# Kernel optimization log

Measured on AMD Instinct MI355X. Metric: run time of the kernel, lower is better.

Reference implementation:

```python
import jax, jax.numpy as jnp
import numpy as np

IN_DIM = 4096
OUT_DIM = 4096
RANK = 8
IN1 = IN2 = OUT1 = OUT2 = 64  # factorize(4096) -> (64, 64)


def setup_inputs() -> dict:
    key = jax.random.key(0)
    k1, k2, k3, k4 = jax.random.split(key, 4)
    x = jax.random.normal(k1, (8, 2048, IN_DIM), dtype=jnp.float32)
    L = jax.random.normal(k2, (OUT1, OUT2, IN1, RANK), dtype=jnp.float32) * 0.05
    R = jax.random.normal(k3, (RANK, OUT2, IN1, IN2), dtype=jnp.float32) * 0.05
    bias = jax.random.normal(k4, (OUT_DIM,), dtype=jnp.float32) * 0.02
    return {"x": x, "L": L, "R": R, "bias": bias}


def reference(x, L, R, bias):
    # Assemble full weight: W[a,b,c,d] = sum_r L[a,b,c,r] * R[r,b,c,d]
    W = jnp.einsum('abcr,rbcd->abcd', L, R).reshape(OUT_DIM, IN_DIM)
    shape = x.shape
    X = x.reshape(-1, IN_DIM)          # [BS, in_dim]
    out = X @ W.T + bias               # addmm(bias, x, W.T)
    return out.reshape(*shape[:-1], OUT_DIM)
```

## Files before the change

kernel.cpp:

```cpp
#include <hip/hip_runtime.h>
#include <hip/hip_bf16.h>

typedef __attribute__((ext_vector_type(8))) short bf16x8;
typedef __attribute__((ext_vector_type(4))) float f32x4;

#define GLDS(g, l) \
  __builtin_amdgcn_global_load_lds((const __attribute__((address_space(1))) void*)(g), \
                                   (__attribute__((address_space(3))) void*)(l), 16, 0, 0)

#define MFMA_BF16 __builtin_amdgcn_mfma_f32_16x16x32_bf16

__global__ __launch_bounds__(256) void k_cvt_bf16(const float* __restrict__ x,
                                                  __hip_bfloat16* __restrict__ y,
                                                  long n8) {
  long stride = (long)gridDim.x * blockDim.x;
  for (long i = (long)blockIdx.x * blockDim.x + threadIdx.x; i < n8; i += stride) {
    const float4* xin = reinterpret_cast<const float4*>(x) + i * 2;
    float4 v0 = xin[0];
    float4 v1 = xin[1];
    union { __hip_bfloat16 h[8]; int4 v; } o;
    o.h[0] = __float2bfloat16(v0.x);
    o.h[1] = __float2bfloat16(v0.y);
    o.h[2] = __float2bfloat16(v0.z);
    o.h[3] = __float2bfloat16(v0.w);
    o.h[4] = __float2bfloat16(v1.x);
    o.h[5] = __float2bfloat16(v1.y);
    o.h[6] = __float2bfloat16(v1.z);
    o.h[7] = __float2bfloat16(v1.w);
    *reinterpret_cast<int4*>(y + i * 8) = o.v;
  }
}

__global__ __launch_bounds__(256) void k_make_w(const float* __restrict__ L,
                                                const float* __restrict__ R,
                                                __hip_bfloat16* __restrict__ W) {
  int o = blockIdx.x;
  int b = o & 63;
  __shared__ float Ls[512];
  Ls[threadIdx.x] = L[(size_t)o * 512 + threadIdx.x];
  Ls[threadIdx.x + 256] = L[(size_t)o * 512 + 256 + threadIdx.x];
  __syncthreads();
  for (int idx = threadIdx.x; idx < 4096; idx += 256) {
    int c = idx >> 6;
    int d = idx & 63;
    float s = 0.f;
#pragma unroll
    for (int r = 0; r < 8; ++r) {
      s += Ls[c * 8 + r] * R[(((size_t)(r * 64 + b) * 64 + c) << 6) + d];
    }
    W[(size_t)o * 4096 + idx] = __float2bfloat16(s);
  }
}

__global__ __launch_bounds__(512, 2) void k_gemm_bt(const __hip_bfloat16* __restrict__ A,
                                                    const __hip_bfloat16* __restrict__ B,
                                                    const float* __restrict__ bias,
                                                    float* __restrict__ C) {
  const int K = 4096, N = 4096, NT = 64;
  __shared__ char lds[131072];
  char* const sAc = lds;
  char* const sBc = lds + 65536;

  const int tid = threadIdx.x;
  const int lane = tid & 63;
  const int wid = tid >> 6;
  const int wr = wid >> 2;
  const int wc = wid & 3;

  const int orig = blockIdx.x;
  const int wg = (orig & 7) * 128 + (orig >> 3);
  const int gm0 = (wg >> 4) * 256;
  const int gn0 = (wg & 15) * 256;

  const int crow = tid >> 3;
  const int scol = ((tid & 7) << 4) ^ ((crow & 7) << 4);
  const int voff = crow * 8192 + scol;
  const int wbase = (tid >> 6) << 10;
  const char* const Ab = (const char*)(A + (size_t)gm0 * K);
  const char* const Bb = (const char*)(B + (size_t)gn0 * K);

#define STAGEA(BUF, TS)                                                      \
  _Pragma("unroll")                                                          \
  for (int j = 0; j < 4; ++j)                                                \
    GLDS(Ab + (size_t)((TS) * 128 + j * 524288) + voff,                      \
         sAc + (BUF) * 32768 + j * 8192 + wbase);

#define STAGEB(BUF, TS)                                                      \
  _Pragma("unroll")                                                          \
  for (int j = 0; j < 4; ++j)                                                \
    GLDS(Bb + (size_t)((TS) * 128 + j * 524288) + voff,                      \
         sBc + (BUF) * 32768 + j * 8192 + wbase);

  const int lr = lane & 15;
  const int lk = lane >> 4;
  const int kx0 = (lk << 4) ^ ((lr & 7) << 4);
  const int kx1 = (64 + (lk << 4)) ^ ((lr & 7) << 4);
  const char* const rA0 = sAc + (((wr << 7) + lr) << 7) + kx0;
  const char* const rA1 = sAc + (((wr << 7) + lr) << 7) + kx1;
  const char* const rB0 = sBc + (((wc << 6) + lr) << 7) + kx0;
  const char* const rB1 = sBc + (((wc << 6) + lr) << 7) + kx1;

#define PREFA(DST, BUF, MOFS)                                                \
  _Pragma("unroll")                                                          \
  for (int m = 0; m < 4; ++m) {                                              \
    DST[m][0] = *(const bf16x8*)(rA0 + (BUF) * 32768 + ((MOFS) + m) * 2048); \
    DST[m][1] = *(const bf16x8*)(rA1 + (BUF) * 32768 + ((MOFS) + m) * 2048); \
  }

#define PREFB(DST, BUF, NOFS)                                                \
  _Pragma("unroll")                                                          \
  for (int n = 0; n < 2; ++n) {                                              \
    DST[n][0] = *(const bf16x8*)(rB0 + (BUF) * 32768 + ((NOFS) + n) * 2048); \
    DST[n][1] = *(const bf16x8*)(rB1 + (BUF) * 32768 + ((NOFS) + n) * 2048); \
  }

#define MFMA8X(AF, BF, MB, NB)                                               \
  _Pragma("unroll")                                                          \
  for (int m = 0; m < 4; ++m) {                                              \
    acc[(MB) + m][(NB) + 0] =                                                \
        MFMA_BF16(AF[m][0], BF[0][0], acc[(MB) + m][(NB) + 0], 0, 0, 0);     \
    acc[(MB) + m][(NB) + 0] =                                                \
        MFMA_BF16(AF[m][1], BF[0][1], acc[(MB) + m][(NB) + 0], 0, 0, 0);     \
    acc[(MB) + m][(NB) + 1] =                                                \
        MFMA_BF16(AF[m][0], BF[1][0], acc[(MB) + m][(NB) + 1], 0, 0, 0);     \
    acc[(MB) + m][(NB) + 1] =                                                \
        MFMA_BF16(AF[m][1], BF[1][1], acc[(MB) + m][(NB) + 1], 0, 0, 0);     \
  }

#define LGKM0 asm volatile("s_waitcnt lgkmcnt(0)" ::: "memory")
#define SBAR0 __builtin_amdgcn_sched_barrier(0)

  f32x4 acc[8][4];
#pragma unroll
  for (int m = 0; m < 8; ++m)
#pragma unroll
    for (int n = 0; n < 4; ++n) acc[m][n] = (f32x4){0.f, 0.f, 0.f, 0.f};

  bf16x8 aX[4][2], aY[4][2], b0[2][2], b2[2][2];

  STAGEA(0, 0) STAGEB(0, 0) STAGEA(1, 1) STAGEB(1, 1)
  asm volatile("s_waitcnt vmcnt(8)" ::: "memory");
  SBAR0;
  __builtin_amdgcn_s_barrier();
  PREFA(aX, 0, 0) PREFB(b0, 0, 0)

#define TILE(BUF, T)                                                         \
  {                                                                          \
    const int tS = ((T) + 2 < NT) ? (T) + 2 : NT - 1;                        \
                                                                     \
    LGKM0; SBAR0;                                                            \
    PREFA(aY, BUF, 4)                                                        \
    SBAR0;                                                                   \
    __builtin_amdgcn_s_setprio(1);                                           \
    MFMA8X(aX, b0, 0, 0)                                                     \
    __builtin_amdgcn_s_setprio(0);                                           \
                                                                     \
    LGKM0; SBAR0;                                                            \
    PREFB(b2, BUF, 2)                                                        \
    SBAR0;                                                                   \
    __builtin_amdgcn_s_setprio(1);                                           \
    MFMA8X(aY, b0, 4, 0)                                                     \
    __builtin_amdgcn_s_setprio(0);                                           \
                                           \
    asm volatile("s_waitcnt lgkmcnt(0) vmcnt(0)" ::: "memory");              \
    SBAR0;                                                                   \
    __builtin_amdgcn_s_barrier();                                            \
    STAGEA(BUF, tS)                                                          \
    PREFB(b0, (BUF) ^ 1, 0)                                                  \
    SBAR0;                                                                   \
    __builtin_amdgcn_s_setprio(1);                                           \
    MFMA8X(aX, b2, 0, 2)                                                     \
    __builtin_amdgcn_s_setprio(0);                                           \
                                           \
    SBAR0;                                                                   \
    STAGEB(BUF, tS)                                                          \
    PREFA(aX, (BUF) ^ 1, 0)                                                  \
    SBAR0;                                                                   \
    __builtin_amdgcn_s_setprio(1);                                           \
    MFMA8X(aY, b2, 4, 2)                                                     \
    __builtin_amdgcn_s_setprio(0);                                           \
  }

  for (int t = 0; t < NT; t += 2) {
    TILE(0, t)
    TILE(1, t + 1)
  }

  const int er = gm0 + (wr << 7) + ((lane >> 4) << 2);
  const int ec = gn0 + (wc << 6) + (lane & 15);
#pragma unroll
  for (int n = 0; n < 4; ++n) {
    const int c = ec + n * 16;
    const float bv = bias[c];
#pragma unroll
    for (int m = 0; m < 8; ++m) {
#pragma unroll
      for (int j = 0; j < 4; ++j) {
        C[(size_t)(er + m * 16 + j) * N + c] = acc[m][n][j] + bv;
      }
    }
  }
}

extern "C" void kernel_launch(void* const* d_in, const int* in_sizes, int n_in,
                              void* d_out, int out_size, void* d_ws, size_t ws_size,
                              hipStream_t stream) {
  const float* x = (const float*)d_in[0];
  const float* L = (const float*)d_in[1];
  const float* R = (const float*)d_in[2];
  const float* bias = (const float*)d_in[3];
  float* out = (float*)d_out;

  __hip_bfloat16* Wb = (__hip_bfloat16*)d_ws;
  __hip_bfloat16* Xb = (__hip_bfloat16*)((char*)d_ws + (size_t)4096 * 4096 * 2);

  const long n8 = (long)16384 * 4096 / 8;
  k_cvt_bf16<<<4096, 256, 0, stream>>>(x, Xb, n8);
  k_make_w<<<4096, 256, 0, stream>>>(L, R, Wb);

  dim3 grid(1024);
  k_gemm_bt<<<grid, 512, 0, stream>>>(Xb, Wb, bias, out);
}
```

Before: 575.8 us.

## Restructure GEMM main loop into four-phase pipeline with split global-to-LDS staging

```diff
diff --git a/kernel.cpp b/kernel.cpp
--- a/kernel.cpp
+++ b/kernel.cpp
@@ -72,24 +72,32 @@
   const int gm0 = (wg >> 4) * 256;
   const int gn0 = (wg & 15) * 256;
 
-  const int crow = tid >> 3;
-  const int scol = ((tid & 7) << 4) ^ ((crow & 7) << 4);
-  const int voff = crow * 8192 + scol;
-  const int wbase = (tid >> 6) << 10;
+  const int sc8 = ((lane & 7) << 4) ^ ((lane >> 3) << 4);
   const char* const Ab = (const char*)(A + (size_t)gm0 * K);
   const char* const Bb = (const char*)(B + (size_t)gn0 * K);
 
-#define STAGEA(BUF, TS)                                                      \
-  _Pragma("unroll")                                                          \
-  for (int j = 0; j < 4; ++j)                                                \
-    GLDS(Ab + (size_t)((TS) * 128 + j * 524288) + voff,                      \
-         sAc + (BUF) * 32768 + j * 8192 + wbase);
-
-#define STAGEB(BUF, TS)                                                      \
-  _Pragma("unroll")                                                          \
-  for (int j = 0; j < 4; ++j)                                                \
-    GLDS(Bb + (size_t)((TS) * 128 + j * 524288) + voff,                      \
-         sBc + (BUF) * 32768 + j * 8192 + wbase);
+  auto STAGE_A = [&](int buf, int kt, int par) {
+#pragma unroll
+    for (int i = 0; i < 2; ++i) {
+      const int u = (wid << 1) + i;
+      const int j = ((u >> 3) << 1) + par;
+      const int rb = u & 7;
+      const int row = (j << 6) + (rb << 3) + (lane >> 3);
+      GLDS(Ab + (size_t)row * 8192 + (size_t)kt * 128 + sc8,
+           sAc + buf * 32768 + j * 8192 + rb * 1024);
+    }
+  };
+  auto STAGE_B = [&](int buf, int kt, int half) {
+#pragma unroll
+    for (int i = 0; i < 2; ++i) {
+      const int u = (wid << 1) + i;
+      const int j = u >> 2;
+      const int rb = u & 3;
+      const int row = (j << 6) + (half << 5) + (rb << 3) + (lane >> 3);
+      GLDS(Bb + (size_t)row * 8192 + (size_t)kt * 128 + sc8,
+           sBc + buf * 32768 + j * 8192 + (half << 12) + (rb << 10));
+    }
+  };
 
   const int lr = lane & 15;
   const int lk = lane >> 4;
@@ -129,6 +137,9 @@
 
 #define LGKM0 asm volatile("s_waitcnt lgkmcnt(0)" ::: "memory")
 #define SBAR0 __builtin_amdgcn_sched_barrier(0)
+#define VMC4 asm volatile("s_waitcnt vmcnt(4)" ::: "memory")
+#define VMC2 asm volatile("s_waitcnt vmcnt(2)" ::: "memory")
+#define VMC0 asm volatile("s_waitcnt vmcnt(0)" ::: "memory")
 
   f32x4 acc[8][4];
 #pragma unroll
@@ -136,55 +147,59 @@
 #pragma unroll
     for (int n = 0; n < 4; ++n) acc[m][n] = (f32x4){0.f, 0.f, 0.f, 0.f};
 
-  bf16x8 aX[4][2], aY[4][2], b0[2][2], b2[2][2];
-
-  STAGEA(0, 0) STAGEB(0, 0) STAGEA(1, 1) STAGEB(1, 1)
-  asm volatile("s_waitcnt vmcnt(8)" ::: "memory");
+  bf16x8 a0[4][2], a1[4][2], bb0[2][2], bb1[2][2];
+
+  STAGE_A(0, 0, 0);
+  STAGE_B(0, 0, 0);
+  STAGE_B(0, 0, 1);
+  STAGE_A(0, 0, 1);
+  VMC0;
   SBAR0;
   __builtin_amdgcn_s_barrier();
-  PREFA(aX, 0, 0) PREFB(b0, 0, 0)
-
-#define TILE(BUF, T)                                                         \
-  {                                                                          \
-    const int tS = ((T) + 2 < NT) ? (T) + 2 : NT - 1;                        \
-                                                                     \
-    LGKM0; SBAR0;                                                            \
-    PREFA(aY, BUF, 4)                                                        \
-    SBAR0;                                                                   \
-    __builtin_amdgcn_s_setprio(1);                                           \
-    MFMA8X(aX, b0, 0, 0)                                                     \
-    __builtin_amdgcn_s_setprio(0);                                           \
-                                                                     \
-    LGKM0; SBAR0;                                                            \
-    PREFB(b2, BUF, 2)                                                        \
-    SBAR0;                                                                   \
-    __builtin_amdgcn_s_setprio(1);                                           \
-    MFMA8X(aY, b0, 4, 0)                                                     \
-    __builtin_amdgcn_s_setprio(0);                                           \
-                                           \
-    asm volatile("s_waitcnt lgkmcnt(0) vmcnt(0)" ::: "memory");              \
-    SBAR0;                                                                   \
-    __builtin_amdgcn_s_barrier();                                            \
-    STAGEA(BUF, tS)                                                          \
-    PREFB(b0, (BUF) ^ 1, 0)                                                  \
-    SBAR0;                                                                   \
-    __builtin_amdgcn_s_setprio(1);                                           \
-    MFMA8X(aX, b2, 0, 2)                                                     \
-    __builtin_amdgcn_s_setprio(0);                                           \
-                                           \
-    SBAR0;                                                                   \
-    STAGEB(BUF, tS)                                                          \
-    PREFA(aX, (BUF) ^ 1, 0)                                                  \
-    SBAR0;                                                                   \
-    __builtin_amdgcn_s_setprio(1);                                           \
-    MFMA8X(aY, b2, 4, 2)                                                     \
-    __builtin_amdgcn_s_setprio(0);                                           \
-  }
-
-  for (int t = 0; t < NT; t += 2) {
-    TILE(0, t)
-    TILE(1, t + 1)
-  }
+
+  for (int t = 0; t < NT; ++t) {
+    const int buf = t & 1, nb = buf ^ 1;
+    const bool more = (t + 1 < NT);
+
+    PREFA(a0, buf, 0) PREFB(bb0, buf, 0)
+    if (more) { STAGE_A(nb, t + 1, 0); VMC4; } else { VMC2; }
+    SBAR0;
+    __builtin_amdgcn_s_barrier();
+    LGKM0; SBAR0;
+    __builtin_amdgcn_s_setprio(1);
+    MFMA8X(a0, bb0, 0, 0)
+    __builtin_amdgcn_s_setprio(0);
+    __builtin_amdgcn_s_barrier();
+
+    PREFB(bb1, buf, 2)
+    if (more) { STAGE_B(nb, t + 1, 0); VMC4; } else { VMC0; }
+    SBAR0;
+    __builtin_amdgcn_s_barrier();
+    LGKM0; SBAR0;
+    __builtin_amdgcn_s_setprio(1);
+    MFMA8X(a0, bb1, 0, 2)
+    __builtin_amdgcn_s_setprio(0);
+    __builtin_amdgcn_s_barrier();
+
+    PREFA(a1, buf, 4)
+    if (more) STAGE_B(nb, t + 1, 1);
+    SBAR0;
+    __builtin_amdgcn_s_barrier();
+    LGKM0; SBAR0;
+    __builtin_amdgcn_s_setprio(1);
+    MFMA8X(a1, bb1, 4, 2)
+    __builtin_amdgcn_s_setprio(0);
+    __builtin_amdgcn_s_barrier();
+
+    if (more) { STAGE_A(nb, t + 1, 1); VMC4; }
+    SBAR0;
+    __builtin_amdgcn_s_barrier();
+    __builtin_amdgcn_s_setprio(1);
+    MFMA8X(a1, bb0, 4, 0)
+    __builtin_amdgcn_s_setprio(0);
+    __builtin_amdgcn_s_barrier();
+  }
+  asm volatile("s_waitcnt vmcnt(0) lgkmcnt(0)" ::: "memory");
 
   const int er = gm0 + (wr << 7) + ((lane >> 4) << 2);
   const int ec = gn0 + (wc << 6) + (lane & 15);
```

New measurement: 602.3 us. +4.6%, slower.
